# Kernel tuning notes

Measured on AMD Instinct MI355X. Metric: run time of the kernel, lower is better.

The kernel has to match this reference:

```python
import jax, jax.numpy as jnp
import numpy as np

BETA = 0.9
THRESHOLD = 1.0


def setup_inputs() -> dict:
    key = jax.random.key(0)
    k1, k2 = jax.random.split(key)
    T, N_IN, N_OUT = 1024, 4096, 4096
    x = jax.random.normal(k1, (T, N_IN), dtype=jnp.float32)
    # fc1 weight initialized uniform[0,1), shape [out, in] like nn.Linear
    W = jax.random.uniform(k2, (N_OUT, N_IN), dtype=jnp.float32)
    return {"x": x, "W": W}


def reference(x, W):
    # Precompute the batched linear projection over all timesteps: [T, N_OUT]
    cur = jnp.einsum('ti,oi->to', x, W)
    mem0 = jnp.zeros((W.shape[0],), dtype=x.dtype)

    def step(mem, c):
        # snntorch Leaky, reset_mechanism='subtract':
        # reset is computed from the PREVIOUS membrane potential (detached)
        reset = (mem > THRESHOLD).astype(mem.dtype)
        mem_new = BETA * mem + c - reset * THRESHOLD
        spk = (mem_new > THRESHOLD).astype(mem.dtype)
        return mem_new, (spk, mem_new)

    _, (spk_rec, mem_rec) = jax.lax.scan(step, mem0, cur)
    return spk_rec, mem_rec
```

## Files before the change

kernel.cpp:

```cpp
#include <hip/hip_runtime.h>
#include <hip/hip_bf16.h>
#include <stdint.h>


typedef __attribute__((ext_vector_type(8))) short bf16x8;
typedef __attribute__((ext_vector_type(4))) float floatx4;

#define T_STEPS 1024
#define N_IN    4096
#define N_OUT   4096

#define BM 128
#define BN 128
#define BKK 64

#define PH_T 128
#define NPH  (T_STEPS / PH_T)
#define NB_N 16
#define TP   130

#define TN ((size_t)T_STEPS * N_OUT)

__device__ __forceinline__ unsigned short f2bf_rne(float f) {
    unsigned int u = __builtin_bit_cast(unsigned int, f);
    unsigned int r = 0x7FFFu + ((u >> 16) & 1u);
    return (unsigned short)((u + r) >> 16);
}

__device__ __forceinline__ float bf2f(unsigned short b) {
    unsigned int u = ((unsigned int)b) << 16;
    return __builtin_bit_cast(float, u);
}

__global__ __launch_bounds__(256) void cvt2_kernel(const float4* __restrict__ inX,
                                                   ushort4* __restrict__ outX, int n4x,
                                                   const float4* __restrict__ inW,
                                                   ushort4* __restrict__ outW, int n4w) {
    int i = blockIdx.x * blockDim.x + threadIdx.x;
    const float4* in;
    ushort4* out;
    int k;
    if (i < n4x) { in = inX; out = outX; k = i; }
    else         { in = inW; out = outW; k = i - n4x; if (k >= n4w) return; }
    float4 v = in[k];
    ushort4 o;
    o.x = f2bf_rne(v.x);
    o.y = f2bf_rne(v.y);
    o.z = f2bf_rne(v.z);
    o.w = f2bf_rne(v.w);
    out[k] = o;
}

__device__ __forceinline__ void gload16(const void* g, void* l) {
    __builtin_amdgcn_global_load_lds((const __attribute__((address_space(1))) void*)g,
                                     (__attribute__((address_space(3))) void*)l,
                                     16, 0, 0);
}

__global__ __launch_bounds__(256) void gemm_bt(const short* __restrict__ A,
                                               const short* __restrict__ B,
                                               unsigned short* __restrict__ Pb,
                                               int kLen) {
    __shared__ short sA[BM * BKK];
    __shared__ short sB[BN * BKK];

    const int tid  = threadIdx.x;
    const int lane = tid & 63;
    const int wv   = tid >> 6;
    const int wm   = (wv & 1) * 64;
    const int wn   = (wv >> 1) * 64;

    const int bid    = blockIdx.x;
    const int z      = bid >> 8;
    const int n_tile = bid & 31;
    const int m_tile = (bid >> 5) & 7;
    const long bm = (long)m_tile * BM;
    const long bn = (long)n_tile * BN;
    const int kBeg = z * kLen;
    const int kEnd = kBeg + kLen;
    unsigned short* __restrict__ Pz = Pb + (size_t)z * TN;

    floatx4 acc[4][4] = {};

    const int srow = tid >> 3;
    const int scol = (tid & 7) * 8;
    const short* gA[4];
    const short* gB[4];
    short* lA[4];
    short* lB[4];
#pragma unroll
    for (int p = 0; p < 4; ++p) {
        gA[p] = A + (bm + p * 32 + srow) * (long)N_IN + scol;
        gB[p] = B + (bn + p * 32 + srow) * (long)N_IN + scol;
        lA[p] = sA + p * 2048 + tid * 8;
        lB[p] = sB + p * 2048 + tid * 8;
    }

    const int fm  = lane & 15;
    const int fko = (lane >> 4) * 8;

    for (int k0 = kBeg; k0 < kEnd; k0 += BKK) {
#pragma unroll
        for (int p = 0; p < 4; ++p) gload16(gA[p] + k0, lA[p]);
#pragma unroll
        for (int p = 0; p < 4; ++p) gload16(gB[p] + k0, lB[p]);
        __syncthreads();

#pragma unroll
        for (int ks = 0; ks < 2; ++ks) {
            bf16x8 af[4], bfr[4];
#pragma unroll
            for (int i = 0; i < 4; ++i)
                af[i] = *(const bf16x8*)(sA + (wm + i * 16 + fm) * 64 + ks * 32 + fko);
#pragma unroll
            for (int j = 0; j < 4; ++j)
                bfr[j] = *(const bf16x8*)(sB + (wn + j * 16 + fm) * 64 + ks * 32 + fko);
#pragma unroll
            for (int i = 0; i < 4; ++i)
#pragma unroll
                for (int j = 0; j < 4; ++j)
                    acc[i][j] = __builtin_amdgcn_mfma_f32_16x16x32_bf16(
                        af[i], bfr[j], acc[i][j], 0, 0, 0);
        }
        __syncthreads();
    }

    const int cn = lane & 15;
    const int cm = (lane >> 4) * 4;
#pragma unroll
    for (int i = 0; i < 4; ++i)
#pragma unroll
        for (int j = 0; j < 4; ++j)
#pragma unroll
            for (int r = 0; r < 4; ++r)
                Pz[(bm + wm + i * 16 + cm + r) * (long)N_OUT + bn + wn + j * 16 + cn] =
                    f2bf_rne(acc[i][j][r]);
}

template <int NPART>
__global__ __launch_bounds__(512) void scan_kernel(const unsigned short* __restrict__ Pb,
                                                   float* __restrict__ out) {
    __shared__ float ringCur[2][NB_N * TP];
    __shared__ float ringMem[2][NB_N * TP];

    const int tid  = threadIdx.x;
    const int wv   = tid >> 6;
    const int lane = tid & 63;
    const int n0   = blockIdx.x * NB_N;

    const int pn = lane & 15;
    const int tr = lane >> 4;

    float mem = 0.0f;

    if (wv < 7) {
        float v[NPART][5];
        int gi[5];
#pragma unroll
        for (int i = 0; i < 5; ++i) {
            int g = wv + 7 * i;
            gi[i] = g;
            if (g < 32) {
                size_t idx = (size_t)(g * 4 + tr) * N_OUT + n0 + pn;
#pragma unroll
                for (int zz = 0; zz < NPART; ++zz)
                    v[zz][i] = bf2f(Pb[(size_t)zz * TN + idx]);
            }
        }
#pragma unroll
        for (int i = 0; i < 5; ++i)
            if (gi[i] < 32) {
                float s = v[0][i];
#pragma unroll
                for (int zz = 1; zz < NPART; ++zz) s += v[zz][i];
                ringCur[0][pn * TP + gi[i] * 4 + tr] = s;
            }
    }
    __syncthreads();

    for (int ph = 0; ph < NPH; ++ph) {
        if (wv < 7) {
            if (ph >= 1) {
                const float* mr = ringMem[(ph - 1) & 1];
                const size_t tb = (size_t)(ph - 1) * PH_T;
                float mv[5];
                int gi[5];
#pragma unroll
                for (int i = 0; i < 5; ++i) {
                    int g = wv + 7 * i;
                    gi[i] = g;
                    if (g < 32) mv[i] = mr[pn * TP + g * 4 + tr];
                }
#pragma unroll
                for (int i = 0; i < 5; ++i)
                    if (gi[i] < 32) {
                        size_t idx = (tb + gi[i] * 4 + tr) * N_OUT + n0 + pn;
                        out[idx]      = mv[i] > 1.0f ? 1.0f : 0.0f;
                        out[TN + idx] = mv[i];
                    }
            }
            if (ph + 1 < NPH) {
                const size_t tb = (size_t)(ph + 1) * PH_T;
                float v[NPART][5];
                int gi[5];
#pragma unroll
                for (int i = 0; i < 5; ++i) {
                    int g = wv + 7 * i;
                    gi[i] = g;
                    if (g < 32) {
                        size_t idx = (tb + g * 4 + tr) * N_OUT + n0 + pn;
#pragma unroll
                        for (int zz = 0; zz < NPART; ++zz)
                            v[zz][i] = bf2f(Pb[(size_t)zz * TN + idx]);
                    }
                }
#pragma unroll
                for (int i = 0; i < 5; ++i)
                    if (gi[i] < 32) {
                        float s = v[0][i];
#pragma unroll
                        for (int zz = 1; zz < NPART; ++zz) s += v[zz][i];
                        ringCur[(ph + 1) & 1][pn * TP + gi[i] * 4 + tr] = s;
                    }
            }
        } else if (lane < 16) {
            const float* base = &ringCur[ph & 1][pn * TP];
            float* mbase = &ringMem[ph & 1][pn * TP];
#pragma unroll
            for (int sub = 0; sub < 4; ++sub) {
                float2 buf[16];
#pragma unroll
                for (int q = 0; q < 16; ++q)
                    buf[q] = *(const float2*)&base[sub * 32 + q * 2];
#pragma unroll
                for (int q = 0; q < 16; ++q) {
                    float rst = mem > 1.0f ? 1.0f : 0.0f;
                    mem = fmaf(0.9f, mem, buf[q].x) - rst;
                    float m0 = mem;
                    rst = mem > 1.0f ? 1.0f : 0.0f;
                    mem = fmaf(0.9f, mem, buf[q].y) - rst;
                    float2 mo; mo.x = m0; mo.y = mem;
                    *(float2*)&mbase[sub * 32 + q * 2] = mo;
                }
            }
        }
        __syncthreads();
    }

    if (wv < 7) {
        const float* mr = ringMem[(NPH - 1) & 1];
        const size_t tb = (size_t)(NPH - 1) * PH_T;
        float mv[5];
        int gi[5];
#pragma unroll
        for (int i = 0; i < 5; ++i) {
            int g = wv + 7 * i;
            gi[i] = g;
            if (g < 32) mv[i] = mr[pn * TP + g * 4 + tr];
        }
#pragma unroll
        for (int i = 0; i < 5; ++i)
            if (gi[i] < 32) {
                size_t idx = (tb + gi[i] * 4 + tr) * N_OUT + n0 + pn;
                out[idx]      = mv[i] > 1.0f ? 1.0f : 0.0f;
                out[TN + idx] = mv[i];
            }
    }
}

extern "C" void kernel_launch(void* const* d_in, const int* in_sizes, int n_in,
                              void* d_out, int out_size, void* d_ws, size_t ws_size,
                              hipStream_t stream) {
    const float* x = (const float*)d_in[0];
    const float* W = (const float*)d_in[1];
    float* out = (float*)d_out;

    char* ws = (char*)d_ws;
    const size_t xbBytes = (size_t)T_STEPS * N_IN * 2;
    const size_t WbBytes = (size_t)N_OUT * N_IN * 2;
    const size_t PBytes  = TN * 2;
    short* xb = (short*)ws;
    short* Wb = (short*)(ws + xbBytes);
    unsigned short* Pb = (unsigned short*)(ws + xbBytes + WbBytes);

    const int S = (ws_size >= xbBytes + WbBytes + 2 * PBytes) ? 2 : 1;

    {
        const int n4x = T_STEPS * N_IN / 4;
        const int n4w = N_OUT * N_IN / 4;
        const int nthr = n4x + n4w;
        cvt2_kernel<<<(nthr + 255) / 256, 256, 0, stream>>>(
            (const float4*)x, (ushort4*)xb, n4x,
            (const float4*)W, (ushort4*)Wb, n4w);
    }

    gemm_bt<<<256 * S, 256, 0, stream>>>(xb, Wb, Pb, N_IN / S);

    if (S == 2) scan_kernel<2><<<N_OUT / NB_N, 512, 0, stream>>>(Pb, out);
    else        scan_kernel<1><<<N_OUT / NB_N, 512, 0, stream>>>(Pb, out);
}
```

Baseline: 181.6 us.

## Replace GEMM with 256x256-tile, 8-wave, double-buffered pipelined MFMA kernel

Swaps the simple 128x128 single-buffered GEMM for a 512-thread kernel using 256x256 tiles, XOR-swizzled LDS, and a ping-pong double buffer. Global-to-LDS loads are interleaved with quarter-tile MFMA groups under explicit waitcnt, barriers and priority hints. Split-K is raised to 4 when the workspace allows, so 256 blocks still fill the GPU. The aim is to hide memory latency and reuse more data per tile, at the price of more register pressure, a larger partial-sum buffer, and a scan that must now reduce four partials.

```diff
diff --git a/kernel.cpp b/kernel.cpp
--- a/kernel.cpp
+++ b/kernel.cpp
@@ -9,10 +9,6 @@
 #define T_STEPS 1024
 #define N_IN    4096
 #define N_OUT   4096
-
-#define BM 128
-#define BN 128
-#define BKK 64
 
 #define PH_T 128
 #define NPH  (T_STEPS / PH_T)
@@ -57,84 +53,170 @@
                                      16, 0, 0);
 }
 
-__global__ __launch_bounds__(256) void gemm_bt(const short* __restrict__ A,
-                                               const short* __restrict__ B,
-                                               unsigned short* __restrict__ Pb,
-                                               int kLen) {
-    __shared__ short sA[BM * BKK];
-    __shared__ short sB[BN * BKK];
+#define SB0()  __builtin_amdgcn_sched_barrier(0)
+#define BARR() __builtin_amdgcn_s_barrier()
+
+__global__ __launch_bounds__(512, 2) void gemm8(const short* __restrict__ A,
+                                                const short* __restrict__ B,
+                                                unsigned short* __restrict__ Pb,
+                                                int kLen) {
+    __shared__ short lds[65536];
 
     const int tid  = threadIdx.x;
     const int lane = tid & 63;
     const int wv   = tid >> 6;
-    const int wm   = (wv & 1) * 64;
-    const int wn   = (wv >> 1) * 64;
-
-    const int bid    = blockIdx.x;
-    const int z      = bid >> 8;
-    const int n_tile = bid & 31;
-    const int m_tile = (bid >> 5) & 7;
-    const long bm = (long)m_tile * BM;
-    const long bn = (long)n_tile * BN;
+    const int wm   = (wv >> 2) * 128;
+    const int wn   = (wv & 3) * 64;
+
+    const int bid  = blockIdx.x;
+    const int z    = bid >> 6;
+    const int tile = bid & 63;
+    const long bm  = (long)(tile >> 4) * 256;
+    const long bn  = (long)(tile & 15) * 256;
     const int kBeg = z * kLen;
-    const int kEnd = kBeg + kLen;
     unsigned short* __restrict__ Pz = Pb + (size_t)z * TN;
-
-    floatx4 acc[4][4] = {};
-
-    const int srow = tid >> 3;
-    const int scol = (tid & 7) * 8;
-    const short* gA[4];
-    const short* gB[4];
-    short* lA[4];
-    short* lB[4];
-#pragma unroll
-    for (int p = 0; p < 4; ++p) {
-        gA[p] = A + (bm + p * 32 + srow) * (long)N_IN + scol;
-        gB[p] = B + (bn + p * 32 + srow) * (long)N_IN + scol;
-        lA[p] = sA + p * 2048 + tid * 8;
-        lB[p] = sB + p * 2048 + tid * 8;
-    }
-
-    const int fm  = lane & 15;
-    const int fko = (lane >> 4) * 8;
-
-    for (int k0 = kBeg; k0 < kEnd; k0 += BKK) {
-#pragma unroll
-        for (int p = 0; p < 4; ++p) gload16(gA[p] + k0, lA[p]);
-#pragma unroll
-        for (int p = 0; p < 4; ++p) gload16(gB[p] + k0, lB[p]);
-        __syncthreads();
-
-#pragma unroll
-        for (int ks = 0; ks < 2; ++ks) {
-            bf16x8 af[4], bfr[4];
-#pragma unroll
-            for (int i = 0; i < 4; ++i)
-                af[i] = *(const bf16x8*)(sA + (wm + i * 16 + fm) * 64 + ks * 32 + fko);
-#pragma unroll
-            for (int j = 0; j < 4; ++j)
-                bfr[j] = *(const bf16x8*)(sB + (wn + j * 16 + fm) * 64 + ks * 32 + fko);
-#pragma unroll
-            for (int i = 0; i < 4; ++i)
-#pragma unroll
-                for (int j = 0; j < 4; ++j)
-                    acc[i][j] = __builtin_amdgcn_mfma_f32_16x16x32_bf16(
-                        af[i], bfr[j], acc[i][j], 0, 0, 0);
-        }
-        __syncthreads();
+    const int NT    = kLen / 64;
+    const int NITER = NT / 2;
+
+    const int srow = lane >> 3;
+    const int scol = ((lane & 7) ^ srow) << 3;
+    const short* aSrc = A + (bm + wv * 8 + srow) * (long)N_IN + kBeg + scol;
+    const short* bSrc = B + (bn + wv * 8 + srow) * (long)N_IN + kBeg + scol;
+    const int ldA = wv * 512;
+    const int ldB = 32768 + wv * 512;
+
+    const int fm    = lane & 15;
+    const int fko   = (lane >> 4) * 8;
+    const int cbase = fko ^ ((fm & 7) << 3);
+
+    floatx4 acc[8][4] = {};
+    bf16x8 af[4][2];
+    bf16x8 bq[2][2][2];
+
+    auto loadA = [&](int b, int qm) {
+#pragma unroll
+        for (int mi = 0; mi < 4; ++mi)
+#pragma unroll
+            for (int ks = 0; ks < 2; ++ks)
+                af[mi][ks] = *(const bf16x8*)(
+                    lds + b * 16384 + (wm + qm * 64 + mi * 16 + fm) * 64 +
+                    (cbase ^ (ks << 5)));
+    };
+    auto loadB = [&](int b, int qn) {
+#pragma unroll
+        for (int nj = 0; nj < 2; ++nj)
+#pragma unroll
+            for (int ks = 0; ks < 2; ++ks)
+                bq[qn][nj][ks] = *(const bf16x8*)(
+                    lds + 32768 + b * 16384 + (wn + qn * 32 + nj * 16 + fm) * 64 +
+                    (cbase ^ (ks << 5)));
+    };
+    auto mfma16 = [&](int qm, int qn) {
+        __builtin_amdgcn_s_setprio(1);
+#pragma unroll
+        for (int ks = 0; ks < 2; ++ks)
+#pragma unroll
+            for (int mi = 0; mi < 4; ++mi)
+#pragma unroll
+                for (int nj = 0; nj < 2; ++nj)
+                    acc[qm * 4 + mi][qn * 2 + nj] =
+                        __builtin_amdgcn_mfma_f32_16x16x32_bf16(
+                            af[mi][ks], bq[qn][nj][ks],
+                            acc[qm * 4 + mi][qn * 2 + nj], 0, 0, 0);
+        __builtin_amdgcn_s_setprio(0);
+    };
+    auto stageA = [&](int b, int h, int t) {
+        const short* s = aSrc + (size_t)(h * 128) * N_IN + t * 64;
+        gload16(s,                    lds + b * 16384 + h * 8192 + ldA);
+        gload16(s + (size_t)64 * N_IN, lds + b * 16384 + h * 8192 + 4096 + ldA);
+    };
+    auto stageB = [&](int b, int h, int t) {
+        const short* s = bSrc + (size_t)(h * 128) * N_IN + t * 64;
+        gload16(s,                    lds + b * 16384 + h * 8192 + ldB);
+        gload16(s + (size_t)64 * N_IN, lds + b * 16384 + h * 8192 + 4096 + ldB);
+    };
+
+    stageA(0, 0, 0); stageA(0, 1, 0);
+    stageB(0, 0, 0); stageB(0, 1, 0);
+    stageB(1, 0, 1); stageB(1, 1, 1);
+    asm volatile("s_waitcnt vmcnt(4)" ::: "memory");
+    SB0();
+    BARR();
+
+    for (int i = 0; i < NITER; ++i) {
+        const int t1 = 2 * i + 1;
+        const int t2 = 2 * i + 2;
+        const int t3 = 2 * i + 3;
+        const bool more = (i + 1 < NITER);
+
+        loadA(0, 0); loadB(0, 0);
+        stageA(1, 0, t1);
+        asm volatile("s_waitcnt lgkmcnt(8)" ::: "memory");
+        SB0(); BARR();
+        asm volatile("s_waitcnt lgkmcnt(0)" ::: "memory"); SB0();
+        mfma16(0, 0);
+        SB0(); BARR();
+
+        loadB(0, 1);
+        stageA(1, 1, t1);
+        SB0(); BARR();
+        asm volatile("s_waitcnt lgkmcnt(0)" ::: "memory"); SB0();
+        mfma16(0, 1);
+        SB0(); BARR();
+
+        loadA(0, 1);
+        if (more) stageB(0, 0, t2);
+        SB0(); BARR();
+        asm volatile("s_waitcnt lgkmcnt(0)" ::: "memory"); SB0();
+        mfma16(1, 0);
+        SB0(); BARR();
+
+        if (more) stageB(0, 1, t2);
+        SB0(); BARR();
+        mfma16(1, 1);
+        if (more) { asm volatile("s_waitcnt vmcnt(4)" ::: "memory"); }
+        else      { asm volatile("s_waitcnt vmcnt(0)" ::: "memory"); }
+        SB0(); BARR();
+
+        loadA(1, 0); loadB(1, 0);
+        if (more) stageA(0, 0, t2);
+        asm volatile("s_waitcnt lgkmcnt(8)" ::: "memory");
+        SB0(); BARR();
+        asm volatile("s_waitcnt lgkmcnt(0)" ::: "memory"); SB0();
+        mfma16(0, 0);
+        SB0(); BARR();
+
+        loadB(1, 1);
+        if (more) stageA(0, 1, t2);
+        SB0(); BARR();
+        asm volatile("s_waitcnt lgkmcnt(0)" ::: "memory"); SB0();
+        mfma16(0, 1);
+        SB0(); BARR();
+
+        loadA(1, 1);
+        if (more) stageB(1, 0, t3);
+        SB0(); BARR();
+        asm volatile("s_waitcnt lgkmcnt(0)" ::: "memory"); SB0();
+        mfma16(1, 0);
+        SB0(); BARR();
+
+        if (more) stageB(1, 1, t3);
+        SB0(); BARR();
+        mfma16(1, 1);
+        if (more) { asm volatile("s_waitcnt vmcnt(4)" ::: "memory"); }
+        SB0(); BARR();
     }
 
     const int cn = lane & 15;
     const int cm = (lane >> 4) * 4;
 #pragma unroll
-    for (int i = 0; i < 4; ++i)
-#pragma unroll
-        for (int j = 0; j < 4; ++j)
+    for (int mi = 0; mi < 8; ++mi)
+#pragma unroll
+        for (int nj = 0; nj < 4; ++nj)
 #pragma unroll
             for (int r = 0; r < 4; ++r)
-                Pz[(bm + wm + i * 16 + cm + r) * (long)N_OUT + bn + wn + j * 16 + cn] =
-                    f2bf_rne(acc[i][j][r]);
+                Pz[(bm + wm + mi * 16 + cm + r) * (long)N_OUT + bn + wn + nj * 16 + cn] =
+                    f2bf_rne(acc[mi][nj][r]);
 }
 
 template <int NPART>
@@ -283,7 +365,9 @@
     short* Wb = (short*)(ws + xbBytes);
     unsigned short* Pb = (unsigned short*)(ws + xbBytes + WbBytes);
 
-    const int S = (ws_size >= xbBytes + WbBytes + 2 * PBytes) ? 2 : 1;
+    int S = 1;
+    if (ws_size >= xbBytes + WbBytes + 4 * PBytes)      S = 4;
+    else if (ws_size >= xbBytes + WbBytes + 2 * PBytes) S = 2;
 
     {
         const int n4x = T_STEPS * N_IN / 4;
@@ -294,8 +378,9 @@
             (const float4*)W, (ushort4*)Wb, n4w);
     }
 
-    gemm_bt<<<256 * S, 256, 0, stream>>>(xb, Wb, Pb, N_IN / S);
-
-    if (S == 2) scan_kernel<2><<<N_OUT / NB_N, 512, 0, stream>>>(Pb, out);
-    else        scan_kernel<1><<<N_OUT / NB_N, 512, 0, stream>>>(Pb, out);
-}
+    gemm8<<<64 * S, 512, 0, stream>>>(xb, Wb, Pb, N_IN / S);
+
+    if (S == 4)      scan_kernel<4><<<N_OUT / NB_N, 512, 0, stream>>>(Pb, out);
+    else if (S == 2) scan_kernel<2><<<N_OUT / NB_N, 512, 0, stream>>>(Pb, out);
+    else             scan_kernel<1><<<N_OUT / NB_N, 512, 0, stream>>>(Pb, out);
+}
```

New measurement: 180.4 us. No clear change (-0.7%).
